# Optimization experiments

Hardware: AMD Instinct MI355X
Metric: run time of the kernel (lower is better)

## Reference

```python
import jax, jax.numpy as jnp
import numpy as np

EPS = 1e-5
K = 32

def _bn(x, g, b, m, v):
    # eval-mode BatchNorm over channel (last) axis
    return (x - m) * jax.lax.rsqrt(v + EPS) * g + b

def _attn_pool(x, sw, sb, mw, mb):
    # x: [B, N, C]; scores softmax over N
    s = jax.nn.softmax(jnp.einsum('bnc,oc->bno', x, sw) + sb, axis=1)  # [B,N,1]
    pooled = jnp.sum(s * x, axis=1)  # [B,C]
    return pooled @ mw.T + mb

def setup_inputs() -> dict:
    key = jax.random.key(0)
    ks = jax.random.split(key, 16)
    B, N, G = 8, 8192, 512
    d = {}
    d['xyz'] = jax.random.normal(ks[0], (B, N, 3), jnp.float32)
    d['center_idx'] = jax.random.randint(ks[1], (B, G), 0, N, jnp.int64)
    s = lambda k, shp, f: (jax.random.normal(k, shp, jnp.float32) * f)
    d['w1'] = s(ks[2], (128, 10), 0.3); d['b1'] = jnp.zeros((128,))
    d['g1'] = jnp.ones((128,)); d['be1'] = jnp.zeros((128,))
    d['m1'] = jnp.zeros((128,)); d['v1'] = jnp.ones((128,))
    d['w2'] = s(ks[3], (256, 128), 0.08); d['b2'] = jnp.zeros((256,))
    d['ap1_sw'] = s(ks[4], (1, 256), 0.06); d['ap1_sb'] = jnp.zeros((1,))
    d['ap1_mw'] = s(ks[5], (256, 256), 0.06); d['ap1_mb'] = jnp.zeros((256,))
    d['w3'] = s(ks[6], (512, 512), 0.04); d['b3'] = jnp.zeros((512,))
    d['g2'] = jnp.ones((512,)); d['be2'] = jnp.zeros((512,))
    d['m2'] = jnp.zeros((512,)); d['v2'] = jnp.ones((512,))
    d['w4'] = s(ks[7], (512, 512), 0.04); d['b4'] = jnp.zeros((512,))
    d['ap2_sw'] = s(ks[8], (1, 512), 0.04); d['ap2_sb'] = jnp.zeros((1,))
    d['ap2_mw'] = s(ks[9], (512, 512), 0.04); d['ap2_mb'] = jnp.zeros((512,))
    return d

def reference(xyz, center_idx, w1, b1, g1, be1, m1, v1, w2, b2,
              ap1_sw, ap1_sb, ap1_mw, ap1_mb, w3, b3, g2, be2, m2, v2,
              w4, b4, ap2_sw, ap2_sb, ap2_mw, ap2_mb):
    B, N, _ = xyz.shape
    G = center_idx.shape[1]
    # center sampling (replaces misc.random_sample with explicit indices)
    center = jnp.take_along_axis(xyz, center_idx[..., None], axis=1)  # [B,G,3]
    # knn: squared pairwise distances, top-k smallest
    d2 = (jnp.sum(center**2, -1)[:, :, None] + jnp.sum(xyz**2, -1)[:, None, :]
          - 2.0 * jnp.einsum('bgc,bnc->bgn', center, xyz))  # [B,G,N]
    _, idx = jax.lax.top_k(-d2, K)  # [B,G,K]
    neighborhood = jax.vmap(lambda pts, i: pts[i])(xyz, idx)  # [B,G,K,3]
    xyz_tile = jnp.broadcast_to(center[:, :, None, :], (B, G, K, 3))
    rel = xyz_tile - neighborhood
    rdist = jnp.sqrt(jnp.sum(rel**2, -1, keepdims=True))
    feat = jnp.concatenate([rdist, rel, xyz_tile, neighborhood], -1)  # [B,G,K,10]
    x = feat.reshape(B * G, K, 10)
    # first_conv: 1x1 convs == per-point linear
    x = jax.nn.relu(_bn(jnp.einsum('bnc,oc->bno', x, w1) + b1, g1, be1, m1, v1))
    x = jnp.einsum('bnc,oc->bno', x, w2) + b2  # [BG,K,256]
    fg = _attn_pool(x, ap1_sw, ap1_sb, ap1_mw, ap1_mb)  # [BG,256]
    x = jnp.concatenate([jnp.broadcast_to(fg[:, None, :], x.shape), x], -1)  # [BG,K,512]
    x = jax.nn.relu(_bn(jnp.einsum('bnc,oc->bno', x, w3) + b3, g2, be2, m2, v2))
    x = jnp.einsum('bnc,oc->bno', x, w4) + b4  # [BG,K,512]
    fg2 = _attn_pool(x, ap2_sw, ap2_sb, ap2_mw, ap2_mb)  # [BG,512]
    return center, fg2.reshape(B, G, 512)
```

## Files before the change

### kernel.cpp

```cpp
#include <hip/hip_runtime.h>
#include <math.h>

#define EPSV 1e-5f

typedef __attribute__((ext_vector_type(8))) short bf16x8;
typedef __attribute__((ext_vector_type(4))) float f32x4;

#define MFMA16(a, b, c) __builtin_amdgcn_mfma_f32_16x16x32_bf16(a, b, c, 0, 0, 0)

__device__ __forceinline__ short f2bf(float x) {
    unsigned u = __float_as_uint(x);
    unsigned r = (u + 0x7fffu + ((u >> 16) & 1u)) >> 16;
    return (short)r;
}
__device__ __forceinline__ float bf2f(short h) {
    return __uint_as_float(((unsigned)(unsigned short)h) << 16);
}
__device__ __forceinline__ void bsplit(float x, short& h, short& l) {
    h = f2bf(x);
    l = f2bf(x - bf2f(h));
}

#define KCAP 2048
__global__ __launch_bounds__(256) void prep_knn(
    const float* __restrict__ xyz, const int* __restrict__ cidx,
    int* __restrict__ knn_idx, float* __restrict__ out_center,
    const float* __restrict__ w2, const float* __restrict__ w3,
    const float* __restrict__ mw1, const float* __restrict__ mw2,
    const float* __restrict__ w4, const float* __restrict__ b4,
    const float* __restrict__ sw2, const float* __restrict__ sb2,
    const float* __restrict__ mb2, const float* __restrict__ mb1,
    const float* __restrict__ b3,
    const float* __restrict__ g1, const float* __restrict__ be1,
    const float* __restrict__ m1, const float* __restrict__ v1,
    const float* __restrict__ g2, const float* __restrict__ be2,
    const float* __restrict__ m2, const float* __restrict__ v2,
    short* __restrict__ w2fh, short* __restrict__ w3fh,
    short* __restrict__ Pfh, short* __restrict__ Pfl,
    short* __restrict__ MTfh, short* __restrict__ MTfl,
    float* __restrict__ sc1, float* __restrict__ sh1,
    float* __restrict__ sc2, float* __restrict__ sh2,
    float* __restrict__ u, float* __restrict__ bb, float* __restrict__ ub,
    float* __restrict__ bc3)
{
    __shared__ __align__(16) char shm[12416];
    int B = blockIdx.x, t = threadIdx.x;
    int lane = t & 63, w = t >> 6;

    if (B < 4096) {
        unsigned* cu = (unsigned*)shm;
        unsigned short* cix = (unsigned short*)(shm + 8192);
        unsigned* Tws = (unsigned*)(shm + 12288);
        unsigned* cntS = (unsigned*)(shm + 12304);
        int g = B, b = g >> 9;
        const float* xb = xyz + (size_t)b * 8192 * 3;
        int ci = cidx[g];
        float cx = xb[ci * 3 + 0], cy = xb[ci * 3 + 1], cz = xb[ci * 3 + 2];
        float c2 = cx * cx + cy * cy + cz * cz;
        if (t < 3) out_center[g * 3 + t] = xb[ci * 3 + t];
        if (t == 0) *cntS = 0;

        const float4* p4 = (const float4*)xb + (size_t)t * 24;
        unsigned ue[32];
        unsigned vmin = 0xffffffffu;
        #pragma unroll
        for (int ii = 0; ii < 8; ++ii) {
            float4 v0 = p4[ii * 3 + 0];
            float4 v1 = p4[ii * 3 + 1];
            float4 v2 = p4[ii * 3 + 2];
            float px[4], py[4], pz[4];
            px[0] = v0.x; py[0] = v0.y; pz[0] = v0.z;
            px[1] = v0.w; py[1] = v1.x; pz[1] = v1.y;
            px[2] = v1.z; py[2] = v1.w; pz[2] = v2.x;
            px[3] = v2.y; py[3] = v2.z; pz[3] = v2.w;
            #pragma unroll
            for (int m = 0; m < 4; ++m) {
                float dx = px[m], dy = py[m], dz = pz[m];
                float n2 = dx * dx + dy * dy + dz * dz;
                float d = c2 + n2 - 2.f * (cx * dx + cy * dy + cz * dz);
                unsigned uu = __float_as_uint(d);
                uu = (uu & 0x80000000u) ? ~uu : (uu | 0x80000000u);
                ue[ii * 4 + m] = uu;
                vmin = min(vmin, uu);
            }
        }
        unsigned v = vmin;
        #pragma unroll
        for (int k = 2; k <= 64; k <<= 1) {
            #pragma unroll
            for (int jj = k >> 1; jj > 0; jj >>= 1) {
                unsigned o = __shfl_xor(v, jj);
                bool dir_asc = ((lane & k) == 0) || (k == 64);
                bool lower = (lane & jj) == 0;
                bool take_min = (lower == dir_asc);
                unsigned mn = min(v, o), mx = max(v, o);
                v = take_min ? mn : mx;
            }
        }
        unsigned Tw = __shfl(v, 31);
        if (lane == 0) Tws[w] = Tw;
        __syncthreads();
        unsigned T = min(min(Tws[0], Tws[1]), min(Tws[2], Tws[3]));
        #pragma unroll
        for (int i = 0; i < 32; ++i) {
            if (ue[i] <= T) {
                unsigned pos = atomicAdd(cntS, 1u);
                if (pos < KCAP) {
                    cu[pos] = ue[i];
                    cix[pos] = (unsigned short)(t * 32 + i);
                }
            }
        }
        __syncthreads();
        int C = (int)min(*cntS, (unsigned)KCAP);
        for (int cc = t; cc < C; cc += 256) {
            unsigned uc = cu[cc];
            unsigned short icd = cix[cc];
            int rank = 0;
            for (int j = 0; j < C; ++j) {
                unsigned uj = cu[j];
                rank += (uj < uc) || (uj == uc && cix[j] < icd);
            }
            if (rank < 32) knn_idx[g * 32 + rank] = (int)icd;
        }
        return;
    }

    if (B < 4352) {
        float* col = (float*)shm;
        int c = B - 4096;
        col[t] = mw1[t * 256 + c];
        __syncthreads();
        int ks = c >> 5, qq = (c >> 3) & 3, jj = c & 7;
        for (int oo = t; oo < 512; oo += 256) {
            float acc = 0.f;
            for (int d = 0; d < 256; ++d) acc += col[d] * w3[oo * 512 + d];
            int ct = oo >> 4;
            size_t idx = ((size_t)(ct * 8 + ks) * 64 + qq * 16 + (oo & 15)) * 8 + jj;
            short h, l; bsplit(acc, h, l);
            Pfh[idx] = h; Pfl[idx] = l;
        }
        return;
    }

    if (B < 4864) {
        float* row = (float*)shm;
        int qq = B - 4352;
        row[t] = mw2[(size_t)qq * 512 + t];
        row[t + 256] = mw2[(size_t)qq * 512 + t + 256];
        __syncthreads();
        float a0 = 0.f, a1 = 0.f;
        for (int o = 0; o < 512; ++o) {
            float m = row[o];
            a0 += m * w4[o * 512 + t];
            a1 += m * w4[o * 512 + t + 256];
        }
        int ct = qq >> 4, nl = qq & 15;
        {
            int k = t;
            size_t i0 = (((size_t)(ct * 16 + (k >> 5))) << 9)
                      | ((((k >> 3) & 3) * 16 + nl) << 3) | (k & 7);
            short h, l; bsplit(a0, h, l);
            MTfh[i0] = h; MTfl[i0] = l;
        }
        {
            int k = t + 256;
            size_t i1 = (((size_t)(ct * 16 + (k >> 5))) << 9)
                      | ((((k >> 3) & 3) * 16 + nl) << 3) | (k & 7);
            short h, l; bsplit(a1, h, l);
            MTfh[i1] = h; MTfl[i1] = l;
        }
        return;
    }

    if (B < 4992) {
        int tid = (B - 4864) * 256 + t;
        {
            int i = tid;
            int j = i & 7, ln = (i >> 3) & 63, rest = i >> 9;
            int ks = rest & 3, ct = rest >> 2;
            int o = ct * 16 + (ln & 15);
            int k = ks * 32 + (ln >> 4) * 8 + j;
            w2fh[i] = f2bf(w2[o * 128 + k]);
        }
        #pragma unroll
        for (int s = 0; s < 4; ++s) {
            int i = tid + s * 32768;
            int j = i & 7, ln = (i >> 3) & 63, rest = i >> 9;
            int ks = rest & 7, ct = rest >> 3;
            int o = ct * 16 + (ln & 15);
            int c = 256 + ks * 32 + (ln >> 4) * 8 + j;
            w3fh[i] = f2bf(w3[o * 512 + c]);
        }
        return;
    }

    if (B < 5056) {
        float* b4s = (float*)shm;
        float* red = (float*)(shm + 2048);
        b4s[t] = b4[t];
        b4s[t + 256] = b4[t + 256];
        __syncthreads();
        int q0 = (B - 4992) * 8;
        for (int i = 0; i < 8; ++i) {
            int q = q0 + i;
            float part = mw2[(size_t)q * 512 + t] * b4s[t]
                       + mw2[(size_t)q * 512 + 256 + t] * b4s[256 + t];
            #pragma unroll
            for (int off = 32; off > 0; off >>= 1) part += __shfl_down(part, off);
            if (lane == 0) red[w] = part;
            __syncthreads();
            if (t == 0) bb[q] = mb2[q] + red[0] + red[1] + red[2] + red[3];
            __syncthreads();
        }
        return;
    }

    if (B < 5120) {
        float* mb1s = (float*)shm;
        float* red = (float*)(shm + 1024);
        mb1s[t] = mb1[t];
        __syncthreads();
        int o0 = (B - 5056) * 8;
        for (int i = 0; i < 8; ++i) {
            int o = o0 + i;
            float part = w3[(size_t)o * 512 + t] * mb1s[t];
            #pragma unroll
            for (int off = 32; off > 0; off >>= 1) part += __shfl_down(part, off);
            if (lane == 0) red[w] = part;
            __syncthreads();
            if (t == 0) bc3[o] = b3[o] + red[0] + red[1] + red[2] + red[3];
            __syncthreads();
        }
        return;
    }

    if (B < 5122) {
        int c = (B - 5120) * 256 + t;
        float acc = 0.f;
        for (int o = 0; o < 512; ++o) acc += sw2[o] * w4[o * 512 + c];
        u[c] = acc;
        return;
    }

    if (t < 128) {
        float s = g1[t] * rsqrtf(v1[t] + EPSV);
        sc1[t] = s; sh1[t] = be1[t] - m1[t] * s;
    }
    {
        float s = g2[t] * rsqrtf(v2[t] + EPSV);
        sc2[t] = s; sh2[t] = be2[t] - m2[t] * s;
        s = g2[t + 256] * rsqrtf(v2[t + 256] + EPSV);
        sc2[t + 256] = s; sh2[t + 256] = be2[t + 256] - m2[t + 256] * s;
    }
    if (t < 64) {
        float part = 0.f;
        #pragma unroll
        for (int i = 0; i < 8; ++i) part += sw2[t * 8 + i] * b4[t * 8 + i];
        #pragma unroll
        for (int off = 32; off > 0; off >>= 1) part += __shfl_down(part, off);
        if (t == 0) ub[0] = sb2[0] + part;
    }
}

__global__ __launch_bounds__(512) void mlp_kernel(
    const float* __restrict__ xyz, const int* __restrict__ cidx,
    const int* __restrict__ knn_idx,
    const float* __restrict__ w1, const float* __restrict__ b1,
    const float* __restrict__ sc1, const float* __restrict__ sh1,
    const short* __restrict__ w2fh,
    const float* __restrict__ b2,
    const float* __restrict__ sw1, const float* __restrict__ sb1,
    const short* __restrict__ Pfh, const short* __restrict__ Pfl,
    const float* __restrict__ bc3,
    const short* __restrict__ w3fh,
    const float* __restrict__ sc2, const float* __restrict__ sh2,
    const float* __restrict__ u, const float* __restrict__ ubp,
    short* __restrict__ yh)
{
    __shared__ __align__(16) char smem[78912];
    short* x1 = (short*)smem;
    short* x2 = (short*)smem;
    short* poolA  = (short*)(smem + 65536);
    float* fgpart = (float*)(smem + 69632);
    float* feat   = (float*)(smem + 65536);
    float* cen  = (float*)(smem + 77824);
    float* scs  = (float*)(smem + 77888);
    float* sms  = (float*)(smem + 78400);

    int gb = blockIdx.x * 4;
    int bq = gb >> 9;
    int t = threadIdx.x;
    int lane = t & 63, wv = t >> 6, q = lane >> 4, r = lane & 15;
    const float* xb = xyz + (size_t)bq * 8192 * 3;

    if (t < 4) {
        int ci = cidx[gb + t];
        cen[t * 3 + 0] = xb[ci * 3 + 0];
        cen[t * 3 + 1] = xb[ci * 3 + 1];
        cen[t * 3 + 2] = xb[ci * 3 + 2];
    }
    if (t < 128) scs[t] = sb1[0];
    __syncthreads();

    if (t < 128) {
        int gg = t >> 5, kk = t & 31;
        int n = knn_idx[(gb + gg) * 32 + kk];
        float cxx = cen[gg * 3 + 0], cyy = cen[gg * 3 + 1], czz = cen[gg * 3 + 2];
        float nx = xb[n * 3 + 0], ny = xb[n * 3 + 1], nz = xb[n * 3 + 2];
        float rx = cxx - nx, ry = cyy - ny, rz = czz - nz;
        float rd = sqrtf(rx * rx + ry * ry + rz * rz);
        float* fr = feat + t * 13;
        fr[0] = rd; fr[1] = rx; fr[2] = ry; fr[3] = rz;
        fr[4] = cxx; fr[5] = cyy; fr[6] = czz;
        fr[7] = nx; fr[8] = ny; fr[9] = nz;
    }
    __syncthreads();

    for (int i = 0; i < 32; ++i) {
        int flat = t + (i << 9);
        int row = flat >> 7, o = flat & 127;
        const float* wr = w1 + o * 10;
        const float* fr = feat + row * 13;
        float acc = b1[o];
        #pragma unroll
        for (int c = 0; c < 10; ++c) acc += fr[c] * wr[c];
        acc = fmaxf(acc * sc1[o] + sh1[o], 0.f);
        x1[row * 128 + (o ^ ((row & 7) << 3))] = f2bf(acc);
    }
    __syncthreads();

    f32x4 acc2[8][2];
    #pragma unroll
    for (int rt = 0; rt < 8; ++rt)
        #pragma unroll
        for (int ctl = 0; ctl < 2; ++ctl) {
            float bv = b2[(wv * 2 + ctl) * 16 + r];
            acc2[rt][ctl] = (f32x4){bv, bv, bv, bv};
        }
    #pragma unroll
    for (int ks = 0; ks < 4; ++ks) {
        bf16x8 af[8];
        #pragma unroll
        for (int rt = 0; rt < 8; ++rt) {
            int row = rt * 16 + r;
            int kk = ks * 32 + q * 8;
            af[rt] = *(const bf16x8*)(x1 + row * 128 + (kk ^ ((row & 7) << 3)));
        }
        #pragma unroll
        for (int ctl = 0; ctl < 2; ++ctl) {
            int ct = wv * 2 + ctl;
            size_t woff = ((size_t)(ct * 4 + ks) * 64 + lane) * 8;
            bf16x8 bh = *(const bf16x8*)(w2fh + woff);
            #pragma unroll
            for (int rt = 0; rt < 8; ++rt)
                acc2[rt][ctl] = MFMA16(af[rt], bh, acc2[rt][ctl]);
        }
    }
    {
        float sw1v[2];
        #pragma unroll
        for (int ctl = 0; ctl < 2; ++ctl) sw1v[ctl] = sw1[(wv * 2 + ctl) * 16 + r];
        #pragma unroll
        for (int rt = 0; rt < 8; ++rt)
            #pragma unroll
            for (int j = 0; j < 4; ++j) {
                float s = sw1v[0] * acc2[rt][0][j] + sw1v[1] * acc2[rt][1][j];
                s += __shfl_xor(s, 1); s += __shfl_xor(s, 2);
                s += __shfl_xor(s, 4); s += __shfl_xor(s, 8);
                if (r == 0) atomicAdd(&scs[rt * 16 + q * 4 + j], s);
            }
    }
    __syncthreads();

    if (wv < 4 && lane < 32) {
        float s = scs[wv * 32 + lane];
        float mx = s;
        mx = fmaxf(mx, __shfl_xor(mx, 16));
        mx = fmaxf(mx, __shfl_xor(mx, 8));
        mx = fmaxf(mx, __shfl_xor(mx, 4));
        mx = fmaxf(mx, __shfl_xor(mx, 2));
        mx = fmaxf(mx, __shfl_xor(mx, 1));
        float e = expf(s - mx);
        float sum = e;
        sum += __shfl_xor(sum, 16);
        sum += __shfl_xor(sum, 8);
        sum += __shfl_xor(sum, 4);
        sum += __shfl_xor(sum, 2);
        sum += __shfl_xor(sum, 1);
        sms[wv * 32 + lane] = e / sum;
    }
    #pragma unroll
    for (int rt = 0; rt < 8; ++rt)
        #pragma unroll
        for (int ctl = 0; ctl < 2; ++ctl) {
            int ch = (wv * 2 + ctl) * 16 + r;
            #pragma unroll
            for (int j = 0; j < 4; ++j) {
                int row = rt * 16 + q * 4 + j;
                x2[row * 256 + (ch ^ ((row & 7) << 3))] = f2bf(acc2[rt][ctl][j]);
            }
        }
    __syncthreads();

    {
        #pragma unroll
        for (int ctl = 0; ctl < 2; ++ctl)
            #pragma unroll
            for (int gg = 0; gg < 4; ++gg) {
                float p = 0.f;
                #pragma unroll
                for (int rr = 0; rr < 2; ++rr) {
                    int rt = gg * 2 + rr;
                    #pragma unroll
                    for (int j = 0; j < 4; ++j)
                        p += sms[rt * 16 + q * 4 + j] * acc2[rt][ctl][j];
                }
                p += __shfl_xor(p, 16);
                p += __shfl_xor(p, 32);
                if (q == 0) {
                    int ch = (wv * 2 + ctl) * 16 + r;
                    short h, l; bsplit(p, h, l);
                    poolA[gg * 256 + (ch ^ (gg << 3))] = h;
                    poolA[(gg + 4) * 256 + (ch ^ ((gg + 4) << 3))] = l;
                }
            }
        if (t < 128) scs[t] = ubp[0];
    }
    __syncthreads();

    {
        f32x4 accP[4];
        #pragma unroll
        for (int ctl = 0; ctl < 4; ++ctl) {
            float init = (q == 0) ? bc3[(wv * 4 + ctl) * 16 + r] : 0.f;
            accP[ctl] = (f32x4){init, init, init, init};
        }
        #pragma unroll
        for (int ks = 0; ks < 8; ++ks) {
            int kk = ks * 32 + q * 8;
            bf16x8 pa;
            if (r < 8) pa = *(const bf16x8*)(poolA + r * 256 + (kk ^ (r << 3)));
            else pa = (bf16x8){0, 0, 0, 0, 0, 0, 0, 0};
            #pragma unroll
            for (int ctl = 0; ctl < 4; ++ctl) {
                size_t woff = ((size_t)((wv * 4 + ctl) * 8 + ks) * 64 + lane) * 8;
                bf16x8 ph = *(const bf16x8*)(Pfh + woff);
                bf16x8 pl = *(const bf16x8*)(Pfl + woff);
                accP[ctl] = MFMA16(pa, pl, accP[ctl]);
                accP[ctl] = MFMA16(pa, ph, accP[ctl]);
            }
        }
        #pragma unroll
        for (int ctl = 0; ctl < 4; ++ctl)
            #pragma unroll
            for (int j = 0; j < 4; ++j) {
                float vsum = accP[ctl][j] + __shfl_xor(accP[ctl][j], 16);
                if (q == 0) fgpart[j * 512 + (wv * 4 + ctl) * 16 + r] = vsum;
            }
    }
    __syncthreads();

    f32x4 acc3[8][4];
    #pragma unroll
    for (int rt = 0; rt < 8; ++rt) {
        int gg = rt >> 1;
        #pragma unroll
        for (int ctl = 0; ctl < 4; ++ctl) {
            float fp = fgpart[gg * 512 + (wv * 4 + ctl) * 16 + r];
            acc3[rt][ctl] = (f32x4){fp, fp, fp, fp};
        }
    }
    #pragma unroll
    for (int ks = 0; ks < 8; ++ks) {
        bf16x8 af[8];
        #pragma unroll
        for (int rt = 0; rt < 8; ++rt) {
            int row = rt * 16 + r;
            int kk = ks * 32 + q * 8;
            af[rt] = *(const bf16x8*)(x2 + row * 256 + (kk ^ ((row & 7) << 3)));
        }
        #pragma unroll
        for (int ctl = 0; ctl < 4; ++ctl) {
            int ct = wv * 4 + ctl;
            size_t woff = ((size_t)(ct * 8 + ks) * 64 + lane) * 8;
            bf16x8 bh = *(const bf16x8*)(w3fh + woff);
            #pragma unroll
            for (int rt = 0; rt < 8; ++rt)
                acc3[rt][ctl] = MFMA16(af[rt], bh, acc3[rt][ctl]);
        }
    }
    float uv[4];
    {
        #pragma unroll
        for (int ctl = 0; ctl < 4; ++ctl) {
            int ch = (wv * 4 + ctl) * 16 + r;
            float s = sc2[ch], sh = sh2[ch];
            uv[ctl] = u[ch];
            #pragma unroll
            for (int rt = 0; rt < 8; ++rt)
                #pragma unroll
                for (int j = 0; j < 4; ++j)
                    acc3[rt][ctl][j] = fmaxf(acc3[rt][ctl][j] * s + sh, 0.f);
        }
        #pragma unroll
        for (int rt = 0; rt < 8; ++rt)
            #pragma unroll
            for (int j = 0; j < 4; ++j) {
                float s = uv[0] * acc3[rt][0][j] + uv[1] * acc3[rt][1][j]
                        + uv[2] * acc3[rt][2][j] + uv[3] * acc3[rt][3][j];
                s += __shfl_xor(s, 1); s += __shfl_xor(s, 2);
                s += __shfl_xor(s, 4); s += __shfl_xor(s, 8);
                if (r == 0) atomicAdd(&scs[rt * 16 + q * 4 + j], s);
            }
    }
    __syncthreads();

    if (wv < 4 && lane < 32) {
        float s = scs[wv * 32 + lane];
        float mx = s;
        mx = fmaxf(mx, __shfl_xor(mx, 16));
        mx = fmaxf(mx, __shfl_xor(mx, 8));
        mx = fmaxf(mx, __shfl_xor(mx, 4));
        mx = fmaxf(mx, __shfl_xor(mx, 2));
        mx = fmaxf(mx, __shfl_xor(mx, 1));
        float e = expf(s - mx);
        float sum = e;
        sum += __shfl_xor(sum, 16);
        sum += __shfl_xor(sum, 8);
        sum += __shfl_xor(sum, 4);
        sum += __shfl_xor(sum, 2);
        sum += __shfl_xor(sum, 1);
        sms[wv * 32 + lane] = e / sum;
    }
    __syncthreads();

    {
        #pragma unroll
        for (int ctl = 0; ctl < 4; ++ctl)
            #pragma unroll
            for (int gg = 0; gg < 4; ++gg) {
                float p = 0.f;
                #pragma unroll
                for (int rr = 0; rr < 2; ++rr) {
                    int rt = gg * 2 + rr;
                    #pragma unroll
                    for (int j = 0; j < 4; ++j)
                        p += sms[rt * 16 + q * 4 + j] * acc3[rt][ctl][j];
                }
                p += __shfl_xor(p, 16);
                p += __shfl_xor(p, 32);
                if (q == 0) {
                    int grow = gb + gg;
                    int ch = (wv * 4 + ctl) * 16 + r;
                    yh[(size_t)grow * 512 + ch] = f2bf(p);
                }
            }
    }
}

__global__ __launch_bounds__(256) void fg2_kernel(
    const short* __restrict__ yh,
    const short* __restrict__ MTfh, const short* __restrict__ MTfl,
    const float* __restrict__ bb, float* __restrict__ out_fg2)
{
    int gbase = blockIdx.x * 16;
    int t = threadIdx.x;
    int lane = t & 63, wv = t >> 6, q = lane >> 4, r = lane & 15;
    f32x4 acc[8];
    #pragma unroll
    for (int ctl = 0; ctl < 8; ++ctl) {
        float bv = bb[(wv * 8 + ctl) * 16 + r];
        acc[ctl] = (f32x4){bv, bv, bv, bv};
    }
    #pragma unroll
    for (int ks = 0; ks < 16; ++ks) {
        bf16x8 af = *(const bf16x8*)(yh + (size_t)(gbase + r) * 512 + ks * 32 + q * 8);
        #pragma unroll
        for (int ctl = 0; ctl < 8; ++ctl) {
            int ct = wv * 8 + ctl;
            size_t woff = ((size_t)(ct * 16 + ks) * 64 + lane) * 8;
            bf16x8 bh = *(const bf16x8*)(MTfh + woff);
            bf16x8 bl = *(const bf16x8*)(MTfl + woff);
            acc[ctl] = MFMA16(af, bl, acc[ctl]);
            acc[ctl] = MFMA16(af, bh, acc[ctl]);
        }
    }
    #pragma unroll
    for (int ctl = 0; ctl < 8; ++ctl) {
        int ch = (wv * 8 + ctl) * 16 + r;
        #pragma unroll
        for (int j = 0; j < 4; ++j) {
            int grow = gbase + q * 4 + j;
            out_fg2[(size_t)grow * 512 + ch] = acc[ctl][j];
        }
    }
}

extern "C" void kernel_launch(void* const* d_in, const int* in_sizes, int n_in,
                              void* d_out, int out_size, void* d_ws, size_t ws_size,
                              hipStream_t stream) {
    const float* xyz  = (const float*)d_in[0];
    const int*   cidx = (const int*)d_in[1];
    const float* w1   = (const float*)d_in[2];
    const float* b1   = (const float*)d_in[3];
    const float* g1   = (const float*)d_in[4];
    const float* be1  = (const float*)d_in[5];
    const float* m1   = (const float*)d_in[6];
    const float* v1   = (const float*)d_in[7];
    const float* w2   = (const float*)d_in[8];
    const float* b2   = (const float*)d_in[9];
    const float* sw1  = (const float*)d_in[10];
    const float* sb1  = (const float*)d_in[11];
    const float* mw1  = (const float*)d_in[12];
    const float* mb1  = (const float*)d_in[13];
    const float* w3   = (const float*)d_in[14];
    const float* b3   = (const float*)d_in[15];
    const float* g2   = (const float*)d_in[16];
    const float* be2  = (const float*)d_in[17];
    const float* m2   = (const float*)d_in[18];
    const float* v2   = (const float*)d_in[19];
    const float* w4   = (const float*)d_in[20];
    const float* b4   = (const float*)d_in[21];
    const float* sw2  = (const float*)d_in[22];
    const float* sb2  = (const float*)d_in[23];
    const float* mw2  = (const float*)d_in[24];
    const float* mb2  = (const float*)d_in[25];

    float* out = (float*)d_out;
    char* ws = (char*)d_ws;
    int*   knn_idx = (int*)(ws + 0);
    short* w2fh = (short*)(ws + 524288);
    short* w3fh = (short*)(ws + 655360);
    short* Pfh  = (short*)(ws + 1179648);
    short* Pfl  = (short*)(ws + 1441792);
    float* bc3  = (float*)(ws + 1703936);
    float* sc1  = (float*)(ws + 1705984);
    float* sh1  = (float*)(ws + 1706496);
    float* sc2  = (float*)(ws + 1707008);
    float* sh2  = (float*)(ws + 1709056);
    float* u    = (float*)(ws + 1711104);
    float* bb   = (float*)(ws + 1713152);
    float* ub   = (float*)(ws + 1715200);
    short* MTfh = (short*)(ws + 1715456);
    short* MTfl = (short*)(ws + 2239744);
    short* yh   = (short*)(ws + 2764032);

    prep_knn<<<5123, 256, 0, stream>>>(xyz, cidx, knn_idx, out,
                                       w2, w3, mw1, mw2, w4, b4, sw2, sb2, mb2, mb1, b3,
                                       g1, be1, m1, v1, g2, be2, m2, v2,
                                       w2fh, w3fh, Pfh, Pfl, MTfh, MTfl,
                                       sc1, sh1, sc2, sh2, u, bb, ub, bc3);
    mlp_kernel<<<1024, 512, 0, stream>>>(xyz, cidx, knn_idx,
                                         w1, b1, sc1, sh1, w2fh, b2,
                                         sw1, sb1, Pfh, Pfl, bc3, w3fh,
                                         sc2, sh2, u, ub, yh);
    fg2_kernel<<<256, 256, 0, stream>>>(yh, MTfh, MTfl, bb, out + 12288);
}
```

Baseline: 365.4 us.

## Move first conv to MFMA and drop low-half bf16 weight splits

Replaces the scalar fp32 first-layer linear with a bf16 MFMA path. The features are split into hi/lo bf16 parts and the padded w1 is pre-packed in the prep kernel, with b1 folded into the BN shift. The Pfl and MTfl low-part weight corrections are removed from the pooled-projection and fg2 GEMMs, halving those MFMAs and weight loads. The fgpart shared-memory round trip and its barrier are replaced by cross-lane shuffles. The main risk is lower accuracy from dropping the weight residuals.

Measured after the change: 336.6 us. 1.09x faster.

```diff
diff --git a/kernel.cpp b/kernel.cpp
--- a/kernel.cpp
+++ b/kernel.cpp
@@ -25,6 +25,7 @@
 __global__ __launch_bounds__(256) void prep_knn(
     const float* __restrict__ xyz, const int* __restrict__ cidx,
     int* __restrict__ knn_idx, float* __restrict__ out_center,
+    const float* __restrict__ w1, const float* __restrict__ b1,
     const float* __restrict__ w2, const float* __restrict__ w3,
     const float* __restrict__ mw1, const float* __restrict__ mw2,
     const float* __restrict__ w4, const float* __restrict__ b4,
@@ -35,10 +36,9 @@
     const float* __restrict__ m1, const float* __restrict__ v1,
     const float* __restrict__ g2, const float* __restrict__ be2,
     const float* __restrict__ m2, const float* __restrict__ v2,
-    short* __restrict__ w2fh, short* __restrict__ w3fh,
-    short* __restrict__ Pfh, short* __restrict__ Pfl,
-    short* __restrict__ MTfh, short* __restrict__ MTfl,
-    float* __restrict__ sc1, float* __restrict__ sh1,
+    short* __restrict__ w1fh, short* __restrict__ w2fh, short* __restrict__ w3fh,
+    short* __restrict__ Pfh, short* __restrict__ MTfh,
+    float* __restrict__ sc1, float* __restrict__ shb1,
     float* __restrict__ sc2, float* __restrict__ sh2,
     float* __restrict__ u, float* __restrict__ bb, float* __restrict__ ub,
     float* __restrict__ bc3)
@@ -137,8 +137,7 @@
             for (int d = 0; d < 256; ++d) acc += col[d] * w3[oo * 512 + d];
             int ct = oo >> 4;
             size_t idx = ((size_t)(ct * 8 + ks) * 64 + qq * 16 + (oo & 15)) * 8 + jj;
-            short h, l; bsplit(acc, h, l);
-            Pfh[idx] = h; Pfl[idx] = l;
+            Pfh[idx] = f2bf(acc);
         }
         return;
     }
@@ -160,15 +159,13 @@
             int k = t;
             size_t i0 = (((size_t)(ct * 16 + (k >> 5))) << 9)
                       | ((((k >> 3) & 3) * 16 + nl) << 3) | (k & 7);
-            short h, l; bsplit(a0, h, l);
-            MTfh[i0] = h; MTfl[i0] = l;
+            MTfh[i0] = f2bf(a0);
         }
         {
             int k = t + 256;
             size_t i1 = (((size_t)(ct * 16 + (k >> 5))) << 9)
                       | ((((k >> 3) & 3) * 16 + nl) << 3) | (k & 7);
-            short h, l; bsplit(a1, h, l);
-            MTfh[i1] = h; MTfl[i1] = l;
+            MTfh[i1] = f2bf(a1);
         }
         return;
     }
@@ -245,7 +242,9 @@
 
     if (t < 128) {
         float s = g1[t] * rsqrtf(v1[t] + EPSV);
-        sc1[t] = s; sh1[t] = be1[t] - m1[t] * s;
+        float sh = be1[t] - m1[t] * s;
+        sc1[t] = s;
+        shb1[t] = b1[t] * s + sh;
     }
     {
         float s = g2[t] * rsqrtf(v2[t] + EPSV);
@@ -253,6 +252,14 @@
         s = g2[t + 256] * rsqrtf(v2[t + 256] + EPSV);
         sc2[t + 256] = s; sh2[t + 256] = be2[t + 256] - m2[t + 256] * s;
     }
+    #pragma unroll
+    for (int s = 0; s < 16; ++s) {
+        int i = t + s * 256;
+        int j = i & 7, ln = (i >> 3) & 63, ct = i >> 9;
+        int o = ct * 16 + (ln & 15);
+        int k = (ln >> 4) * 8 + j;
+        w1fh[i] = (k < 10) ? f2bf(w1[o * 10 + k]) : (short)0;
+    }
     if (t < 64) {
         float part = 0.f;
         #pragma unroll
@@ -266,27 +273,26 @@
 __global__ __launch_bounds__(512) void mlp_kernel(
     const float* __restrict__ xyz, const int* __restrict__ cidx,
     const int* __restrict__ knn_idx,
-    const float* __restrict__ w1, const float* __restrict__ b1,
-    const float* __restrict__ sc1, const float* __restrict__ sh1,
+    const short* __restrict__ w1fh,
+    const float* __restrict__ sc1, const float* __restrict__ shb1,
     const short* __restrict__ w2fh,
     const float* __restrict__ b2,
     const float* __restrict__ sw1, const float* __restrict__ sb1,
-    const short* __restrict__ Pfh, const short* __restrict__ Pfl,
-    const float* __restrict__ bc3,
+    const short* __restrict__ Pfh, const float* __restrict__ bc3,
     const short* __restrict__ w3fh,
     const float* __restrict__ sc2, const float* __restrict__ sh2,
     const float* __restrict__ u, const float* __restrict__ ubp,
     short* __restrict__ yh)
 {
-    __shared__ __align__(16) char smem[78912];
+    __shared__ __align__(16) char smem[70784];
     short* x1 = (short*)smem;
     short* x2 = (short*)smem;
+    short* feat_h = (short*)(smem + 32768);
+    short* feat_l = (short*)(smem + 40960);
     short* poolA  = (short*)(smem + 65536);
-    float* fgpart = (float*)(smem + 69632);
-    float* feat   = (float*)(smem + 65536);
-    float* cen  = (float*)(smem + 77824);
-    float* scs  = (float*)(smem + 77888);
-    float* sms  = (float*)(smem + 78400);
+    float* cen  = (float*)(smem + 69632);
+    float* scs  = (float*)(smem + 69696);
+    float* sms  = (float*)(smem + 70208);
 
     int gb = blockIdx.x * 4;
     int bq = gb >> 9;
@@ -310,23 +316,45 @@
         float nx = xb[n * 3 + 0], ny = xb[n * 3 + 1], nz = xb[n * 3 + 2];
         float rx = cxx - nx, ry = cyy - ny, rz = czz - nz;
         float rd = sqrtf(rx * rx + ry * ry + rz * rz);
-        float* fr = feat + t * 13;
-        fr[0] = rd; fr[1] = rx; fr[2] = ry; fr[3] = rz;
-        fr[4] = cxx; fr[5] = cyy; fr[6] = czz;
-        fr[7] = nx; fr[8] = ny; fr[9] = nz;
-    }
-    __syncthreads();
-
-    for (int i = 0; i < 32; ++i) {
-        int flat = t + (i << 9);
-        int row = flat >> 7, o = flat & 127;
-        const float* wr = w1 + o * 10;
-        const float* fr = feat + row * 13;
-        float acc = b1[o];
-        #pragma unroll
-        for (int c = 0; c < 10; ++c) acc += fr[c] * wr[c];
-        acc = fmaxf(acc * sc1[o] + sh1[o], 0.f);
-        x1[row * 128 + (o ^ ((row & 7) << 3))] = f2bf(acc);
+        float f[10];
+        f[0] = rd; f[1] = rx; f[2] = ry; f[3] = rz;
+        f[4] = cxx; f[5] = cyy; f[6] = czz;
+        f[7] = nx; f[8] = ny; f[9] = nz;
+        short* fh = feat_h + t * 32;
+        short* fl = feat_l + t * 32;
+        #pragma unroll
+        for (int c = 0; c < 10; ++c) {
+            short h, l; bsplit(f[c], h, l);
+            fh[c] = h; fl[c] = l;
+        }
+        #pragma unroll
+        for (int c = 10; c < 32; ++c) { fh[c] = 0; fl[c] = 0; }
+    }
+    __syncthreads();
+
+    {
+        f32x4 acc1[8];
+        #pragma unroll
+        for (int rt = 0; rt < 8; ++rt) acc1[rt] = (f32x4){0.f, 0.f, 0.f, 0.f};
+        bf16x8 bw = *(const bf16x8*)(w1fh + ((size_t)wv * 64 + lane) * 8);
+        #pragma unroll
+        for (int rt = 0; rt < 8; ++rt) {
+            int row = rt * 16 + r;
+            bf16x8 ah = *(const bf16x8*)(feat_h + row * 32 + q * 8);
+            bf16x8 al = *(const bf16x8*)(feat_l + row * 32 + q * 8);
+            acc1[rt] = MFMA16(al, bw, acc1[rt]);
+            acc1[rt] = MFMA16(ah, bw, acc1[rt]);
+        }
+        int o = wv * 16 + r;
+        float s1v = sc1[o], sbv = shb1[o];
+        #pragma unroll
+        for (int rt = 0; rt < 8; ++rt)
+            #pragma unroll
+            for (int j = 0; j < 4; ++j) {
+                int row = rt * 16 + q * 4 + j;
+                float vv = fmaxf(acc1[rt][j] * s1v + sbv, 0.f);
+                x1[row * 128 + (o ^ ((row & 7) << 3))] = f2bf(vv);
+            }
     }
     __syncthreads();
 
@@ -429,13 +457,12 @@
     }
     __syncthreads();
 
+    float fgv[4][4];
+    float bc3v[4];
     {
         f32x4 accP[4];
         #pragma unroll
-        for (int ctl = 0; ctl < 4; ++ctl) {
-            float init = (q == 0) ? bc3[(wv * 4 + ctl) * 16 + r] : 0.f;
-            accP[ctl] = (f32x4){init, init, init, init};
-        }
+        for (int ctl = 0; ctl < 4; ++ctl) accP[ctl] = (f32x4){0.f, 0.f, 0.f, 0.f};
         #pragma unroll
         for (int ks = 0; ks < 8; ++ks) {
             int kk = ks * 32 + q * 8;
@@ -446,20 +473,21 @@
             for (int ctl = 0; ctl < 4; ++ctl) {
                 size_t woff = ((size_t)((wv * 4 + ctl) * 8 + ks) * 64 + lane) * 8;
                 bf16x8 ph = *(const bf16x8*)(Pfh + woff);
-                bf16x8 pl = *(const bf16x8*)(Pfl + woff);
-                accP[ctl] = MFMA16(pa, pl, accP[ctl]);
                 accP[ctl] = MFMA16(pa, ph, accP[ctl]);
             }
         }
         #pragma unroll
-        for (int ctl = 0; ctl < 4; ++ctl)
+        for (int ctl = 0; ctl < 4; ++ctl) {
+            bc3v[ctl] = bc3[(wv * 4 + ctl) * 16 + r];
             #pragma unroll
             for (int j = 0; j < 4; ++j) {
-                float vsum = accP[ctl][j] + __shfl_xor(accP[ctl][j], 16);
-                if (q == 0) fgpart[j * 512 + (wv * 4 + ctl) * 16 + r] = vsum;
-            }
-    }
-    __syncthreads();
+                float x = accP[ctl][j];
+                x += __shfl_xor(x, 16);
+                x += __shfl_xor(x, 32);
+                fgv[ctl][j] = x;
+            }
+        }
+    }
 
     f32x4 acc3[8][4];
     #pragma unroll
@@ -467,7 +495,7 @@
         int gg = rt >> 1;
         #pragma unroll
         for (int ctl = 0; ctl < 4; ++ctl) {
-            float fp = fgpart[gg * 512 + (wv * 4 + ctl) * 16 + r];
+            float fp = fgv[ctl][gg] + bc3v[ctl];
             acc3[rt][ctl] = (f32x4){fp, fp, fp, fp};
         }
     }
@@ -561,7 +589,7 @@
 
 __global__ __launch_bounds__(256) void fg2_kernel(
     const short* __restrict__ yh,
-    const short* __restrict__ MTfh, const short* __restrict__ MTfl,
+    const short* __restrict__ MTfh,
     const float* __restrict__ bb, float* __restrict__ out_fg2)
 {
     int gbase = blockIdx.x * 16;
@@ -581,8 +609,6 @@
             int ct = wv * 8 + ctl;
             size_t woff = ((size_t)(ct * 16 + ks) * 64 + lane) * 8;
             bf16x8 bh = *(const bf16x8*)(MTfh + woff);
-            bf16x8 bl = *(const bf16x8*)(MTfl + woff);
-            acc[ctl] = MFMA16(af, bl, acc[ctl]);
             acc[ctl] = MFMA16(af, bh, acc[ctl]);
         }
     }
@@ -633,27 +659,27 @@
     short* w2fh = (short*)(ws + 524288);
     short* w3fh = (short*)(ws + 655360);
     short* Pfh  = (short*)(ws + 1179648);
-    short* Pfl  = (short*)(ws + 1441792);
+    short* w1fh = (short*)(ws + 1441792);
     float* bc3  = (float*)(ws + 1703936);
     float* sc1  = (float*)(ws + 1705984);
-    float* sh1  = (float*)(ws + 1706496);
+    float* shb1 = (float*)(ws + 1706496);
     float* sc2  = (float*)(ws + 1707008);
     float* sh2  = (float*)(ws + 1709056);
     float* u    = (float*)(ws + 1711104);
     float* bb   = (float*)(ws + 1713152);
     float* ub   = (float*)(ws + 1715200);
     short* MTfh = (short*)(ws + 1715456);
-    short* MTfl = (short*)(ws + 2239744);
     short* yh   = (short*)(ws + 2764032);
 
     prep_knn<<<5123, 256, 0, stream>>>(xyz, cidx, knn_idx, out,
-                                       w2, w3, mw1, mw2, w4, b4, sw2, sb2, mb2, mb1, b3,
+                                       w1, b1, w2, w3, mw1, mw2, w4, b4, sw2, sb2,
+                                       mb2, mb1, b3,
                                        g1, be1, m1, v1, g2, be2, m2, v2,
-                                       w2fh, w3fh, Pfh, Pfl, MTfh, MTfl,
-                                       sc1, sh1, sc2, sh2, u, bb, ub, bc3);
+                                       w1fh, w2fh, w3fh, Pfh, MTfh,
+                                       sc1, shb1, sc2, sh2, u, bb, ub, bc3);
     mlp_kernel<<<1024, 512, 0, stream>>>(xyz, cidx, knn_idx,
-                                         w1, b1, sc1, sh1, w2fh, b2,
-                                         sw1, sb1, Pfh, Pfl, bc3, w3fh,
+                                         w1fh, sc1, shb1, w2fh, b2,
+                                         sw1, sb1, Pfh, bc3, w3fh,
                                          sc2, sh2, u, ub, yh);
-    fg2_kernel<<<256, 256, 0, stream>>>(yh, MTfh, MTfl, bb, out + 12288);
+    fg2_kernel<<<256, 256, 0, stream>>>(yh, MTfh, bb, out + 12288);
 }
```
